# Kernel optimization log

Hardware: AMD Instinct MI355X
Metric: run time of the kernel (lower is better)

Reference implementation:

```python
import jax, jax.numpy as jnp
import numpy as np

B, T, C = 2, 2048, 2048
NH, NKV = 16, 4
HD = C // NH  # 128


def setup_inputs() -> dict:
    key = jax.random.key(0)
    ks = jax.random.split(key, 5)
    w = lambda k, shape: jax.random.normal(k, shape, jnp.float32) * 0.02
    return {
        "x": jax.random.normal(ks[0], (B, T, C), jnp.float32),
        "Wq": w(ks[1], (C, C)),
        "Wk": w(ks[2], (C, NKV * HD)),
        "Wv": w(ks[3], (C, NKV * HD)),
        "Wproj": w(ks[4], (C, C)),
    }


def _rope(x):
    # x: [B, H, T, D]; rotate-half RoPE with base 10000
    D = x.shape[-1]
    t = x.shape[-2]
    inv_freq = 1.0 / (10000.0 ** (jnp.arange(0, D, 2, dtype=jnp.float32) / D))
    freqs = jnp.arange(t, dtype=jnp.float32)[:, None] * inv_freq[None, :]  # [T, D/2]
    emb = jnp.concatenate([freqs, freqs], axis=-1)  # [T, D]
    cos, sin = jnp.cos(emb), jnp.sin(emb)
    x1, x2 = x[..., : D // 2], x[..., D // 2 :]
    rotated = jnp.concatenate([-x2, x1], axis=-1)
    return x * cos + rotated * sin


def reference(x, Wq, Wk, Wv, Wproj):
    b, t, c = x.shape
    q = (x @ Wq).reshape(b, t, NH, HD).transpose(0, 2, 1, 3)    # [B,NH,T,HD]
    k = (x @ Wk).reshape(b, t, NKV, HD).transpose(0, 2, 1, 3)   # [B,NKV,T,HD]
    v = (x @ Wv).reshape(b, t, NKV, HD).transpose(0, 2, 1, 3)
    q = _rope(q)
    k = _rope(k)
    rep = NH // NKV
    k = jnp.repeat(k, rep, axis=1)  # [B,NH,T,HD]
    v = jnp.repeat(v, rep, axis=1)
    scale = 1.0 / jnp.sqrt(jnp.float32(HD))
    scores = jnp.einsum("bhqd,bhkd->bhqk", q, k) * scale        # [B,NH,T,T]
    causal = jnp.tril(jnp.ones((t, t), dtype=bool))
    scores = jnp.where(causal, scores, jnp.finfo(scores.dtype).min)
    attn = jax.nn.softmax(scores, axis=-1)
    y = jnp.einsum("bhqk,bhkd->bhqd", attn, v)                  # [B,NH,T,HD]
    y = y.transpose(0, 2, 1, 3).reshape(b, t, c)
    return y @ Wproj
```

## Files before the change

### kernel.cpp

```cpp
#include <hip/hip_runtime.h>

#define B_ 2
#define T_ 2048
#define C_ 2048
#define NH_ 16
#define NKV_ 4
#define HD_ 128
#define M_ 4096
#define NQKV_ 3072

typedef __bf16 bf16x8 __attribute__((ext_vector_type(8)));
typedef float f32x4 __attribute__((ext_vector_type(4)));
typedef float f32x16 __attribute__((ext_vector_type(16)));

__device__ __forceinline__ unsigned short f2bf(float f) {
  union { float f; unsigned u; } c{f};
  unsigned u = c.u + 0x7FFFu + ((c.u >> 16) & 1u);
  return (unsigned short)(u >> 16);
}

#define GLOAD_LDS16(g, l)                                        \
  __builtin_amdgcn_global_load_lds(                              \
      (const __attribute__((address_space(1))) void*)(g),        \
      (__attribute__((address_space(3))) void*)(l), 16, 0, 0)

__device__ __forceinline__ bf16x8 ldsread128(const unsigned short* p) {
  uint4 d;
  asm volatile("ds_read_b128 %0, %1"
               : "=v"(d)
               : "v"((const __attribute__((address_space(3))) void*)p));
  union { uint4 u; bf16x8 v; } c;
  c.u = d;
  return c.v;
}

__global__ void rope_table_kernel(float2* __restrict__ rt) {
  int t = blockIdx.x, i = threadIdx.x;
  float inv = powf(10000.f, -(float)(2 * i) / 128.f);
  float s, c;
  sincosf((float)t * inv, &s, &c);
  rt[t * 64 + i] = make_float2(c, s);
}

__global__ void convx_kernel(const float* __restrict__ x, unsigned short* __restrict__ xb, int n4) {
  int i = blockIdx.x * blockDim.x + threadIdx.x;
  if (i >= n4) return;
  float4 v = reinterpret_cast<const float4*>(x)[i];
  union { ushort4 u; unsigned short s[4]; } o;
  o.s[0] = f2bf(v.x); o.s[1] = f2bf(v.y); o.s[2] = f2bf(v.z); o.s[3] = f2bf(v.w);
  reinterpret_cast<ushort4*>(xb)[i] = o.u;
}

__global__ void transpose_conv4_kernel(const float* __restrict__ Wq, const float* __restrict__ Wk,
                                       const float* __restrict__ Wv, const float* __restrict__ Wp,
                                       unsigned short* __restrict__ wt) {
  __shared__ float tile[32][33];
  int id = blockIdx.x;
  const float* W;
  unsigned short* Wt;
  int N, bx, by;
  if (id < 4096)      { W = Wq; Wt = wt;                          N = 2048; int u = id;        bx = u & 63; by = u >> 6; }
  else if (id < 5120) { W = Wk; Wt = wt + (size_t)2048 * 2048;    N = 512;  int u = id - 4096; bx = u & 15; by = u >> 4; }
  else if (id < 6144) { W = Wv; Wt = wt + (size_t)2560 * 2048;    N = 512;  int u = id - 5120; bx = u & 15; by = u >> 4; }
  else                { W = Wp; Wt = wt + (size_t)3072 * 2048;    N = 2048; int u = id - 6144; bx = u & 63; by = u >> 6; }
  const int K = 2048;
  bx *= 32; by *= 32;
  int tx = threadIdx.x & 31, ty = threadIdx.x >> 5;
#pragma unroll
  for (int r = 0; r < 32; r += 8)
    tile[ty + r][tx] = W[(size_t)(by + ty + r) * N + bx + tx];
  __syncthreads();
#pragma unroll
  for (int r = 0; r < 32; r += 8)
    Wt[(size_t)(bx + ty + r) * K + by + tx] = f2bf(tile[tx][ty + r]);
}

__global__ void transpose_v_kernel(const unsigned short* __restrict__ qkv,
                                   unsigned short* __restrict__ vt) {
  __shared__ unsigned short tile[32][33];
  int bh = blockIdx.z;
  int b = bh >> 2, kvh = bh & 3;
  int t0 = blockIdx.x * 32, d0 = blockIdx.y * 32;
  int tx = threadIdx.x & 31, ty = threadIdx.x >> 5;
#pragma unroll
  for (int r = 0; r < 32; r += 8)
    tile[ty + r][tx] = qkv[(size_t)(b * T_ + t0 + ty + r) * NQKV_ + 2560 + kvh * HD_ + d0 + tx];
  __syncthreads();
#pragma unroll
  for (int r = 0; r < 32; r += 8)
    vt[(size_t)(bh * HD_ + d0 + ty + r) * T_ + t0 + tx] = tile[tx][ty + r];
}

template <int BM, typename OUT, bool ROPE>
__global__ __launch_bounds__(512, 1) void gemm8p(const unsigned short* __restrict__ A,
                                                 const unsigned short* __restrict__ Bt,
                                                 OUT* __restrict__ Cm,
                                                 const float2* __restrict__ rt,
                                                 int M, int N, int K) {
  constexpr int MR = BM / 64;
  __shared__ __align__(16) unsigned short As[2][2][BM * 32];
  __shared__ __align__(16) unsigned short Bs[2][2][256 * 32];
  int tid = threadIdx.x, wid = tid >> 6, lane = tid & 63;
  int l15 = lane & 15, l4 = lane >> 4;
  int wr = wid >> 1, wc = wid & 1;
  size_t arow0 = (size_t)blockIdx.y * BM;
  size_t brow0 = (size_t)blockIdx.x * 256;
  int tmax = K / 64 - 1;

  f32x4 acc[MR][8];
#pragma unroll
  for (int m = 0; m < MR; ++m)
#pragma unroll
    for (int n = 0; n < 8; ++n) acc[m][n] = (f32x4){0.f, 0.f, 0.f, 0.f};

  auto stageA = [&](int slot, int kh, int tile) {
    int k0 = tile * 64 + kh * 32;
    constexpr int NLD = (BM * 32 * 2) / (512 * 16);
#pragma unroll
    for (int i = 0; i < NLD; ++i) {
      int c = i * 512 + wid * 64 + lane;
      int rg = c >> 2, cg = (c & 3) ^ (rg & 3);
      const unsigned short* g = A + (arow0 + rg) * K + k0 + cg * 8;
      GLOAD_LDS16(g, &As[slot][kh][c * 8]);
    }
  };
  auto stageB = [&](int slot, int kh, int tile) {
    int k0 = tile * 64 + kh * 32;
#pragma unroll
    for (int i = 0; i < 2; ++i) {
      int c = i * 512 + wid * 64 + lane;
      int rg = c >> 2, cg = (c & 3) ^ (rg & 3);
      const unsigned short* g = Bt + (brow0 + rg) * K + k0 + cg * 8;
      GLOAD_LDS16(g, &Bs[slot][kh][c * 8]);
    }
  };

  stageA(0, 0, 0); stageB(0, 0, 0); stageA(0, 1, 0); stageB(0, 1, 0);
  stageA(1, 0, 1); stageB(1, 0, 1); stageA(1, 1, 1);
  if constexpr (BM == 256) asm volatile("s_waitcnt vmcnt(6)" ::: "memory");
  else                     asm volatile("s_waitcnt vmcnt(4)" ::: "memory");
  __builtin_amdgcn_s_barrier();

  int NT2 = K / 128;
  for (int it = 0; it < NT2; ++it) {
    int t2 = it * 2;
#pragma unroll
    for (int tt = 0; tt < 2; ++tt) {
      bf16x8 af[MR];
#pragma unroll
      for (int kh = 0; kh < 2; ++kh) {
#pragma unroll
        for (int nh = 0; nh < 2; ++nh) {
          int p = tt * 4 + kh * 2 + nh + 1;
          if (nh == 0) {
#pragma unroll
            for (int m = 0; m < MR; ++m) {
              int r = wr * (MR * 16) + m * 16 + l15;
              af[m] = ldsread128(&As[tt][kh][r * 32 + ((l4 ^ (r & 3)) * 8)]);
            }
          }
          bf16x8 bf[4];
#pragma unroll
          for (int j = 0; j < 4; ++j) {
            int r = wc * 128 + (nh * 4 + j) * 16 + l15;
            bf[j] = ldsread128(&Bs[tt][kh][r * 32 + ((l4 ^ (r & 3)) * 8)]);
          }
          if (p == 1) stageB(1, 1, t2 + 1);
          if (p == 2) stageA(0, 0, t2 + 2 <= tmax ? t2 + 2 : tmax);
          if (p == 3) stageB(0, 0, t2 + 2 <= tmax ? t2 + 2 : tmax);
          if (p == 4) stageA(0, 1, t2 + 2 <= tmax ? t2 + 2 : tmax);
          if (p == 5) stageB(0, 1, t2 + 2 <= tmax ? t2 + 2 : tmax);
          if (p == 6) stageA(1, 0, t2 + 3 <= tmax ? t2 + 3 : tmax);
          if (p == 7) stageB(1, 0, t2 + 3 <= tmax ? t2 + 3 : tmax);
          if (p == 8) stageA(1, 1, t2 + 3 <= tmax ? t2 + 3 : tmax);

          __builtin_amdgcn_s_barrier();
          asm volatile("s_waitcnt lgkmcnt(0)" ::: "memory");
          __builtin_amdgcn_sched_barrier(0);
          __builtin_amdgcn_s_setprio(1);
#pragma unroll
          for (int m = 0; m < MR; ++m)
#pragma unroll
            for (int j = 0; j < 4; ++j)
              acc[m][nh * 4 + j] = __builtin_amdgcn_mfma_f32_16x16x32_bf16(
                  af[m], bf[j], acc[m][nh * 4 + j], 0, 0, 0);
          __builtin_amdgcn_s_setprio(0);
          if (p == 4 || p == 8) {
            if constexpr (BM == 256) asm volatile("s_waitcnt vmcnt(6)" ::: "memory");
            else                     asm volatile("s_waitcnt vmcnt(4)" ::: "memory");
          }
          __builtin_amdgcn_s_barrier();
        }
      }
    }
  }

  bool dorope = ROPE && (brow0 + wc * 128 < 2560);
#pragma unroll
  for (int m = 0; m < MR; ++m)
#pragma unroll
    for (int r = 0; r < 4; ++r) {
      size_t row = arow0 + wr * (MR * 16) + m * 16 + l4 * 4 + r;
      if (dorope) {
        int t = (int)(row & (T_ - 1));
#pragma unroll
        for (int n = 0; n < 4; ++n) {
          float2 cs = rt[t * 64 + n * 16 + l15];
          float a1 = acc[m][n][r], a2 = acc[m][n + 4][r];
          size_t col = brow0 + wc * 128 + n * 16 + l15;
          Cm[row * N + col]      = f2bf(a1 * cs.x - a2 * cs.y);
          Cm[row * N + col + 64] = f2bf(a2 * cs.x + a1 * cs.y);
        }
      } else {
#pragma unroll
        for (int n = 0; n < 8; ++n) {
          size_t col = brow0 + wc * 128 + n * 16 + l15;
          float v = acc[m][n][r];
          if constexpr (sizeof(OUT) == 4) Cm[row * N + col] = v;
          else                            Cm[row * N + col] = f2bf(v);
        }
      }
    }
}

__global__ __launch_bounds__(256, 2) void attn_kernel(const unsigned short* __restrict__ qkv,
                                                      const unsigned short* __restrict__ vt,
                                                      unsigned short* __restrict__ att) {
  constexpr int KB = 64;
  __shared__ __align__(16) unsigned short Kl[2][KB * 128];
  __shared__ __align__(16) unsigned short Vl[2][128 * KB];
  int tid = threadIdx.x, w = tid >> 6, lane = tid & 63;
  int l31 = lane & 31, hi = lane >> 5;
  int h4 = hi * 4;

  int id = blockIdx.x;
  int u = id & 255, half = id >> 8;
  int bh = u & 31;
  int qh = u >> 5;
  int qi = half ? (15 - qh) : qh;
  int q0 = qi * 128;
  int b = bh >> 4, hd = bh & 15, kvh = hd >> 2;
  int qr0 = q0 + w * 32;
  int ql = qr0 + l31;

  bf16x8 qf[8];
  {
    const unsigned short* qb = qkv + (size_t)(b * T_ + ql) * NQKV_ + hd * HD_ + hi * 8;
    const float scale = 0.08838834764831845f * 1.4426950408889634f;
#pragma unroll
    for (int df = 0; df < 8; ++df) {
      bf16x8 t = *reinterpret_cast<const bf16x8*>(qb + df * 16);
#pragma unroll
      for (int j = 0; j < 8; ++j) t[j] = (__bf16)((float)t[j] * scale);
      qf[df] = t;
    }
  }

  f32x16 o[4];
#pragma unroll
  for (int dt = 0; dt < 4; ++dt)
#pragma unroll
    for (int r = 0; r < 16; ++r) o[dt][r] = 0.f;
  float mr = -1e30f, lr = 0.f;

  auto stage = [&](int buf, int kv0) {
#pragma unroll
    for (int i = 0; i < 4; ++i) {
      int c = (i * 4 + w) * 64 + lane;
      int g = c ^ ((c >> 4) & 7);
      const unsigned short* src =
          qkv + (size_t)(b * T_ + kv0 + (g >> 4)) * NQKV_ + C_ + kvh * HD_ + (g & 15) * 8;
      GLOAD_LDS16(src, &Kl[buf][(i * 4 + w) * 512]);
    }
#pragma unroll
    for (int i = 0; i < 4; ++i) {
      int c = (i * 4 + w) * 64 + lane;
      int g = c ^ ((c >> 3) & 7);
      const unsigned short* src =
          vt + (size_t)((b * NKV_ + kvh) * HD_ + (g >> 3)) * T_ + kv0 + (g & 7) * 8;
      GLOAD_LDS16(src, &Vl[buf][(i * 4 + w) * 512]);
    }
  };

  int nt = q0 / KB + 2;
  stage(0, 0);
  __syncthreads();
  int cur = 0;
  for (int kt = 0; kt < nt; ++kt) {
    int kv0 = kt * KB;
    if (kt + 1 < nt) stage(cur ^ 1, kv0 + KB);

    if (kv0 <= qr0 + 31) {
      f32x16 s[2];
#pragma unroll
      for (int r = 0; r < 16; ++r) { s[0][r] = 0.f; s[1][r] = 0.f; }
      const unsigned short* Kb = &Kl[cur][0];
      __builtin_amdgcn_s_setprio(1);
#pragma unroll
      for (int t2 = 0; t2 < 2; ++t2)
#pragma unroll
        for (int df = 0; df < 8; ++df) {
          bf16x8 kf = *reinterpret_cast<const bf16x8*>(
              Kb + (((t2 * 32 + l31) * 128 + df * 16 + hi * 8) ^ ((l31 & 7) << 3)));
          s[t2] = __builtin_amdgcn_mfma_f32_32x32x16_bf16(kf, qf[df], s[t2], 0, 0, 0);
        }
      __builtin_amdgcn_s_setprio(0);

      float rm = -1e30f;
      if ((kv0 + KB - 1) > qr0) {
#pragma unroll
        for (int t2 = 0; t2 < 2; ++t2)
#pragma unroll
          for (int r = 0; r < 16; ++r) {
            float sv = s[t2][r];
            int kcol = kv0 + t2 * 32 + (r & 3) + 8 * (r >> 2) + h4;
            if (kcol > ql) sv = -1e30f;
            s[t2][r] = sv;
            rm = fmaxf(rm, sv);
          }
      } else {
#pragma unroll
        for (int t2 = 0; t2 < 2; ++t2)
#pragma unroll
          for (int r = 0; r < 16; ++r) rm = fmaxf(rm, s[t2][r]);
      }
      rm = fmaxf(rm, __shfl_xor(rm, 32));

      if (!__all(rm <= mr + 11.0f)) {
        float mnew = fmaxf(mr, rm);
        float alpha = exp2f(mr - mnew);
        mr = mnew;
        lr *= alpha;
#pragma unroll
        for (int dt = 0; dt < 4; ++dt)
#pragma unroll
          for (int r = 0; r < 16; ++r) o[dt][r] *= alpha;
      }

      float ps = 0.f;
#pragma unroll
      for (int t2 = 0; t2 < 2; ++t2)
#pragma unroll
        for (int r = 0; r < 16; ++r) {
          float p = exp2f(s[t2][r] - mr);
          s[t2][r] = p;
          ps += p;
        }
      lr += ps;

      unsigned pk[2][8];
#pragma unroll
      for (int t2 = 0; t2 < 2; ++t2)
#pragma unroll
        for (int i = 0; i < 8; ++i) {
          union { unsigned u32; __bf16 hh[2]; } pr;
          pr.hh[0] = (__bf16)s[t2][2 * i];
          pr.hh[1] = (__bf16)s[t2][2 * i + 1];
          pk[t2][i] = pr.u32;
        }

      bf16x8 pb[4];
#pragma unroll
      for (int f = 0; f < 4; ++f) {
        int t2 = f >> 1, bq = (f & 1) * 4;
        union { bf16x8 v; unsigned d[4]; } fr;
#pragma unroll
        for (int p = 0; p < 2; ++p) {
          unsigned uu = pk[t2][bq + p];
          unsigned ww = pk[t2][bq + 2 + p];
          unsigned us = (unsigned)__shfl_xor((int)uu, 32);
          unsigned ws = (unsigned)__shfl_xor((int)ww, 32);
          fr.d[p]     = hi ? ws : uu;
          fr.d[2 + p] = hi ? ww : us;
        }
        pb[f] = fr.v;
      }

      const unsigned short* Vb = &Vl[cur][0];
      __builtin_amdgcn_s_setprio(1);
#pragma unroll
      for (int dt = 0; dt < 4; ++dt)
#pragma unroll
        for (int kf = 0; kf < 4; ++kf) {
          bf16x8 vf = *reinterpret_cast<const bf16x8*>(
              Vb + (((dt * 32 + l31) * KB + kf * 16 + hi * 8) ^ ((l31 & 7) << 3)));
          o[dt] = __builtin_amdgcn_mfma_f32_32x32x16_bf16(vf, pb[kf], o[dt], 0, 0, 0);
        }
      __builtin_amdgcn_s_setprio(0);
    }

    __syncthreads();
    cur ^= 1;
  }

  float ls = lr + __shfl_xor(lr, 32);
  float inv = 1.f / ls;
  unsigned short* ob = att + (size_t)(b * T_ + ql) * C_ + hd * HD_;
#pragma unroll
  for (int dt = 0; dt < 4; ++dt)
#pragma unroll
    for (int r = 0; r < 16; ++r) {
      int d = dt * 32 + (r & 3) + 8 * (r >> 2) + h4;
      ob[d] = f2bf(o[dt][r] * inv);
    }
}

extern "C" void kernel_launch(void* const* d_in, const int* in_sizes, int n_in,
                              void* d_out, int out_size, void* d_ws, size_t ws_size,
                              hipStream_t stream) {
  const float* x  = (const float*)d_in[0];
  const float* Wq = (const float*)d_in[1];
  const float* Wk = (const float*)d_in[2];
  const float* Wv = (const float*)d_in[3];
  const float* Wp = (const float*)d_in[4];
  float* out = (float*)d_out;
  char* ws = (char*)d_ws;

  unsigned short* xb  = (unsigned short*)(ws);
  unsigned short* wt  = (unsigned short*)(ws + 16777216);
  unsigned short* qkv = (unsigned short*)(ws + 37748736);
  float2*         rt  = (float2*)(ws + 62914560);
  unsigned short* vt  = (unsigned short*)(ws + 63963136);
  unsigned short* att = xb;

  rope_table_kernel<<<T_, 64, 0, stream>>>(rt);
  convx_kernel<<<(M_ * C_ / 4 + 255) / 256, 256, 0, stream>>>(x, xb, M_ * C_ / 4);
  transpose_conv4_kernel<<<dim3(10240), 256, 0, stream>>>(Wq, Wk, Wv, Wp, wt);

  gemm8p<256, unsigned short, true><<<dim3(NQKV_ / 256, M_ / 256), 512, 0, stream>>>(
      xb, wt, qkv, rt, M_, NQKV_, C_);
  transpose_v_kernel<<<dim3(T_ / 32, HD_ / 32, B_ * NKV_), 256, 0, stream>>>(qkv, vt);
  attn_kernel<<<dim3(512), 256, 0, stream>>>(qkv, vt, att);
  gemm8p<128, float, false><<<dim3(C_ / 256, M_ / 128), 512, 0, stream>>>(
      att, wt + (size_t)3072 * 2048, out, nullptr, M_, C_, C_);
}
```

Measured before the change: 215.7 us.

## Split KV range for long causal query tiles and merge prep kernels

The longest causal query tiles (qi 10–15) are now split into two blocks, each covering half of the KV range. Each half writes an unnormalized partial output plus its running max and sum, and a new combine kernel merges them with log-sum-exp weights. The goal is to balance work across CUs and shorten the tail of the attention launch, at the cost of extra partial-output traffic and one more launch. Separately, the rope-table, x-conversion and weight-transpose kernels are fused into a single prep launch to cut launch overhead. The partial buffers reuse workspace regions (the Wq/Wk/Wv transposes and the rope table) that are dead by then.

```diff
diff --git a/kernel.cpp b/kernel.cpp
--- a/kernel.cpp
+++ b/kernel.cpp
@@ -18,6 +18,10 @@
   unsigned u = c.u + 0x7FFFu + ((c.u >> 16) & 1u);
   return (unsigned short)(u >> 16);
 }
+__device__ __forceinline__ float bf2f(unsigned short h) {
+  union { unsigned u; float f; } c{(unsigned)h << 16};
+  return c.f;
+}
 
 #define GLOAD_LDS16(g, l)                                        \
   __builtin_amdgcn_global_load_lds(                              \
@@ -34,45 +38,44 @@
   return c.v;
 }
 
-__global__ void rope_table_kernel(float2* __restrict__ rt) {
-  int t = blockIdx.x, i = threadIdx.x;
-  float inv = powf(10000.f, -(float)(2 * i) / 128.f);
-  float s, c;
-  sincosf((float)t * inv, &s, &c);
-  rt[t * 64 + i] = make_float2(c, s);
-}
-
-__global__ void convx_kernel(const float* __restrict__ x, unsigned short* __restrict__ xb, int n4) {
-  int i = blockIdx.x * blockDim.x + threadIdx.x;
-  if (i >= n4) return;
-  float4 v = reinterpret_cast<const float4*>(x)[i];
-  union { ushort4 u; unsigned short s[4]; } o;
-  o.s[0] = f2bf(v.x); o.s[1] = f2bf(v.y); o.s[2] = f2bf(v.z); o.s[3] = f2bf(v.w);
-  reinterpret_cast<ushort4*>(xb)[i] = o.u;
-}
-
-__global__ void transpose_conv4_kernel(const float* __restrict__ Wq, const float* __restrict__ Wk,
-                                       const float* __restrict__ Wv, const float* __restrict__ Wp,
-                                       unsigned short* __restrict__ wt) {
-  __shared__ float tile[32][33];
+__global__ void prep_kernel(const float* __restrict__ x, const float* __restrict__ Wq,
+                            const float* __restrict__ Wk, const float* __restrict__ Wv,
+                            const float* __restrict__ Wp, unsigned short* __restrict__ xb,
+                            unsigned short* __restrict__ wt, float2* __restrict__ rt) {
   int id = blockIdx.x;
-  const float* W;
-  unsigned short* Wt;
-  int N, bx, by;
-  if (id < 4096)      { W = Wq; Wt = wt;                          N = 2048; int u = id;        bx = u & 63; by = u >> 6; }
-  else if (id < 5120) { W = Wk; Wt = wt + (size_t)2048 * 2048;    N = 512;  int u = id - 4096; bx = u & 15; by = u >> 4; }
-  else if (id < 6144) { W = Wv; Wt = wt + (size_t)2560 * 2048;    N = 512;  int u = id - 5120; bx = u & 15; by = u >> 4; }
-  else                { W = Wp; Wt = wt + (size_t)3072 * 2048;    N = 2048; int u = id - 6144; bx = u & 63; by = u >> 6; }
-  const int K = 2048;
-  bx *= 32; by *= 32;
-  int tx = threadIdx.x & 31, ty = threadIdx.x >> 5;
-#pragma unroll
-  for (int r = 0; r < 32; r += 8)
-    tile[ty + r][tx] = W[(size_t)(by + ty + r) * N + bx + tx];
-  __syncthreads();
-#pragma unroll
-  for (int r = 0; r < 32; r += 8)
-    Wt[(size_t)(bx + ty + r) * K + by + tx] = f2bf(tile[tx][ty + r]);
+  if (id < 10240) {
+    __shared__ float tile[32][33];
+    const float* W;
+    unsigned short* Wt;
+    int N, bx, by;
+    if (id < 4096)      { W = Wq; Wt = wt;                       N = 2048; int u = id;        bx = u & 63; by = u >> 6; }
+    else if (id < 5120) { W = Wk; Wt = wt + (size_t)2048 * 2048; N = 512;  int u = id - 4096; bx = u & 15; by = u >> 4; }
+    else if (id < 6144) { W = Wv; Wt = wt + (size_t)2560 * 2048; N = 512;  int u = id - 5120; bx = u & 15; by = u >> 4; }
+    else                { W = Wp; Wt = wt + (size_t)3072 * 2048; N = 2048; int u = id - 6144; bx = u & 63; by = u >> 6; }
+    const int K = 2048;
+    bx *= 32; by *= 32;
+    int tx = threadIdx.x & 31, ty = threadIdx.x >> 5;
+#pragma unroll
+    for (int r = 0; r < 32; r += 8)
+      tile[ty + r][tx] = W[(size_t)(by + ty + r) * N + bx + tx];
+    __syncthreads();
+#pragma unroll
+    for (int r = 0; r < 32; r += 8)
+      Wt[(size_t)(bx + ty + r) * K + by + tx] = f2bf(tile[tx][ty + r]);
+  } else if (id < 18432) {
+    int i = (id - 10240) * 256 + threadIdx.x;
+    float4 v = reinterpret_cast<const float4*>(x)[i];
+    union { ushort4 u; unsigned short s[4]; } o;
+    o.s[0] = f2bf(v.x); o.s[1] = f2bf(v.y); o.s[2] = f2bf(v.z); o.s[3] = f2bf(v.w);
+    reinterpret_cast<ushort4*>(xb)[i] = o.u;
+  } else {
+    int g = (id - 18432) * 256 + threadIdx.x;
+    int t = g >> 6, i = g & 63;
+    float inv = powf(10000.f, -(float)(2 * i) / 128.f);
+    float s, c;
+    sincosf((float)t * inv, &s, &c);
+    rt[t * 64 + i] = make_float2(c, s);
+  }
 }
 
 __global__ void transpose_v_kernel(const unsigned short* __restrict__ qkv,
@@ -225,7 +228,9 @@
 
 __global__ __launch_bounds__(256, 2) void attn_kernel(const unsigned short* __restrict__ qkv,
                                                       const unsigned short* __restrict__ vt,
-                                                      unsigned short* __restrict__ att) {
+                                                      unsigned short* __restrict__ att,
+                                                      unsigned short* __restrict__ pO,
+                                                      float2* __restrict__ ml) {
   constexpr int KB = 64;
   __shared__ __align__(16) unsigned short Kl[2][KB * 128];
   __shared__ __align__(16) unsigned short Vl[2][128 * KB];
@@ -234,10 +239,20 @@
   int h4 = hi * 4;
 
   int id = blockIdx.x;
-  int u = id & 255, half = id >> 8;
-  int bh = u & 31;
-  int qh = u >> 5;
-  int qi = half ? (15 - qh) : qh;
+  int qi, bh, kt0, kt1, slot = -1;
+  if (id < 64) {
+    qi = 9 - (id >> 5); bh = id & 31; kt0 = 0; kt1 = 2 * qi + 2;
+  } else if (id < 448) {
+    int s = id - 64;
+    int pairidx = s >> 1, hihalf = s & 1;
+    qi = 15 - (pairidx >> 5); bh = pairidx & 31;
+    int nt = 2 * qi + 2, h = nt >> 1;
+    kt0 = hihalf ? h : 0; kt1 = hihalf ? nt : h;
+    slot = s;
+  } else {
+    int u = id - 448;
+    qi = 7 - (u >> 5); bh = u & 31; kt0 = 0; kt1 = 2 * qi + 2;
+  }
   int q0 = qi * 128;
   int b = bh >> 4, hd = bh & 15, kvh = hd >> 2;
   int qr0 = q0 + w * 32;
@@ -282,13 +297,12 @@
     }
   };
 
-  int nt = q0 / KB + 2;
-  stage(0, 0);
+  stage(0, kt0 * KB);
   __syncthreads();
   int cur = 0;
-  for (int kt = 0; kt < nt; ++kt) {
+  for (int kt = kt0; kt < kt1; ++kt) {
     int kv0 = kt * KB;
-    if (kt + 1 < nt) stage(cur ^ 1, kv0 + KB);
+    if (kt + 1 < kt1) stage(cur ^ 1, kv0 + KB);
 
     if (kv0 <= qr0 + 31) {
       f32x16 s[2];
@@ -394,15 +408,58 @@
   }
 
   float ls = lr + __shfl_xor(lr, 32);
-  float inv = 1.f / ls;
-  unsigned short* ob = att + (size_t)(b * T_ + ql) * C_ + hd * HD_;
-#pragma unroll
-  for (int dt = 0; dt < 4; ++dt)
-#pragma unroll
-    for (int r = 0; r < 16; ++r) {
-      int d = dt * 32 + (r & 3) + 8 * (r >> 2) + h4;
-      ob[d] = f2bf(o[dt][r] * inv);
-    }
+  if (slot < 0) {
+    float inv = 1.f / ls;
+    unsigned short* ob = att + (size_t)(b * T_ + ql) * C_ + hd * HD_;
+#pragma unroll
+    for (int dt = 0; dt < 4; ++dt)
+#pragma unroll
+      for (int r = 0; r < 16; ++r) {
+        int d = dt * 32 + (r & 3) + 8 * (r >> 2) + h4;
+        ob[d] = f2bf(o[dt][r] * inv);
+      }
+  } else {
+    int lrow = w * 32 + l31;
+    unsigned short* po = pO + (size_t)slot * 16384 + lrow * 128;
+#pragma unroll
+    for (int dt = 0; dt < 4; ++dt)
+#pragma unroll
+      for (int r = 0; r < 16; ++r) {
+        int d = dt * 32 + (r & 3) + 8 * (r >> 2) + h4;
+        po[d] = f2bf(o[dt][r]);
+      }
+    if (hi == 0) ml[slot * 128 + lrow] = make_float2(mr, ls);
+  }
+}
+
+__global__ void combine_kernel(const unsigned short* __restrict__ pO,
+                               const float2* __restrict__ ml,
+                               unsigned short* __restrict__ att) {
+  int pairidx = blockIdx.x;
+  int qi = 15 - (pairidx >> 5), bh = pairidx & 31;
+  int b = bh >> 4, hd = bh & 15;
+  int q0 = qi * 128;
+  int s0 = pairidx * 2, s1 = s0 + 1;
+  int tid = threadIdx.x;
+  int row = tid >> 1, dh = (tid & 1) * 64;
+  float2 ml0 = ml[s0 * 128 + row], ml1 = ml[s1 * 128 + row];
+  float m = fmaxf(ml0.x, ml1.x);
+  float w0 = exp2f(ml0.x - m), w1 = exp2f(ml1.x - m);
+  float inv = 1.f / (w0 * ml0.y + w1 * ml1.y);
+  const unsigned short* p0 = pO + (size_t)s0 * 16384 + row * 128 + dh;
+  const unsigned short* p1 = pO + (size_t)s1 * 16384 + row * 128 + dh;
+  unsigned short* ob = att + (size_t)(b * T_ + q0 + row) * C_ + hd * HD_ + dh;
+#pragma unroll
+  for (int j = 0; j < 64; j += 4) {
+    ushort4 a = *reinterpret_cast<const ushort4*>(p0 + j);
+    ushort4 c = *reinterpret_cast<const ushort4*>(p1 + j);
+    ushort4 r;
+    r.x = f2bf((w0 * bf2f(a.x) + w1 * bf2f(c.x)) * inv);
+    r.y = f2bf((w0 * bf2f(a.y) + w1 * bf2f(c.y)) * inv);
+    r.z = f2bf((w0 * bf2f(a.z) + w1 * bf2f(c.z)) * inv);
+    r.w = f2bf((w0 * bf2f(a.w) + w1 * bf2f(c.w)) * inv);
+    *reinterpret_cast<ushort4*>(ob + j) = r;
+  }
 }
 
 extern "C" void kernel_launch(void* const* d_in, const int* in_sizes, int n_in,
@@ -422,15 +479,16 @@
   float2*         rt  = (float2*)(ws + 62914560);
   unsigned short* vt  = (unsigned short*)(ws + 63963136);
   unsigned short* att = xb;
-
-  rope_table_kernel<<<T_, 64, 0, stream>>>(rt);
-  convx_kernel<<<(M_ * C_ / 4 + 255) / 256, 256, 0, stream>>>(x, xb, M_ * C_ / 4);
-  transpose_conv4_kernel<<<dim3(10240), 256, 0, stream>>>(Wq, Wk, Wv, Wp, wt);
+  unsigned short* pO  = wt;
+  float2*         ml  = rt;
+
+  prep_kernel<<<dim3(18944), 256, 0, stream>>>(x, Wq, Wk, Wv, Wp, xb, wt, rt);
 
   gemm8p<256, unsigned short, true><<<dim3(NQKV_ / 256, M_ / 256), 512, 0, stream>>>(
       xb, wt, qkv, rt, M_, NQKV_, C_);
   transpose_v_kernel<<<dim3(T_ / 32, HD_ / 32, B_ * NKV_), 256, 0, stream>>>(qkv, vt);
-  attn_kernel<<<dim3(512), 256, 0, stream>>>(qkv, vt, att);
+  attn_kernel<<<dim3(704), 256, 0, stream>>>(qkv, vt, att, pO, ml);
+  combine_kernel<<<dim3(192), 256, 0, stream>>>(pO, ml, att);
   gemm8p<128, float, false><<<dim3(C_ / 256, M_ / 128), 512, 0, stream>>>(
       att, wt + (size_t)3072 * 2048, out, nullptr, M_, C_, C_);
 }
```

Result: no change. 214.0 us, median of 2 (-0.8%).
